# Kernel tuning notes

Measured on AMD Instinct MI355X. Metric: run time of the kernel, lower is better.

## Reference

```python
import jax, jax.numpy as jnp
import numpy as np

HEAD_DIM = 128
NUM_HEADS = 16
NUM_KV_HEADS = 16
ROPE_MAX_POS = 4096
ROPE_BASE = 10000.0


def _rope_tables(seq_len):
    # cos/sin cached tables: [S, D/2]
    inv_freq = 1.0 / (ROPE_BASE ** (jnp.arange(0, HEAD_DIM, 2, dtype=jnp.float32) / HEAD_DIM))
    t = jnp.arange(seq_len, dtype=jnp.float32)
    freqs = jnp.outer(t, inv_freq)
    return jnp.cos(freqs), jnp.sin(freqs)


def _apply_rope(x, cos, sin):
    # x: [B, S, H, D]; cos/sin: [S, D/2] -> broadcast over heads as [S, 1, D/2]
    orig_dtype = x.dtype
    c = cos[:, None, :]
    s = sin[:, None, :]
    xf = x.astype(jnp.float32)
    x_real, x_im = jnp.split(xf, 2, axis=-1)  # half-split (not interleaved) RoPE
    x_real_e = x_real * c - x_im * s
    x_im_e = x_im * c + x_real * s
    return jnp.concatenate((x_real_e, x_im_e), axis=-1).astype(orig_dtype)


def setup_inputs() -> dict:
    key = jax.random.key(0)
    k1, k2, k3 = jax.random.split(key, 3)
    B, S, H = 1, 4096, 2048
    hidden_states = jax.random.normal(k1, (B, S, H), dtype=jnp.float32)
    # trunc-normal-ish init, std ~ 1/sqrt(fan_in)
    w_qkv = jax.random.normal(k2, ((NUM_HEADS + 2 * NUM_KV_HEADS) * HEAD_DIM, H), dtype=jnp.float32) / jnp.sqrt(jnp.float32(H))
    w_o = jax.random.normal(k3, (H, NUM_HEADS * HEAD_DIM), dtype=jnp.float32) / jnp.sqrt(jnp.float32(NUM_HEADS * HEAD_DIM))
    return {"hidden_states": hidden_states, "w_qkv": w_qkv, "w_o": w_o}


def reference(hidden_states, w_qkv, w_o):
    B, S, _ = hidden_states.shape
    qkv = jnp.einsum('bsh,oh->bso', hidden_states, w_qkv)
    qkv = qkv.reshape(B, S, NUM_HEADS + 2 * NUM_KV_HEADS, HEAD_DIM)
    q = qkv[:, :, :NUM_HEADS]
    k = qkv[:, :, NUM_HEADS:NUM_HEADS + NUM_KV_HEADS]
    v = qkv[:, :, NUM_HEADS + NUM_KV_HEADS:]

    cos, sin = _rope_tables(S)
    q = _apply_rope(q, cos, sin)
    k = _apply_rope(k, cos, sin)

    scale = 1.0 / jnp.sqrt(jnp.float32(HEAD_DIM)).astype(q.dtype)
    # scores: [B, H, Sq, Sk]
    scores = jnp.einsum('bqhd,bkhd->bhqk', q, k) * scale
    causal = jnp.tril(jnp.ones((S, S), dtype=bool))
    scores = jnp.where(causal[None, None], scores, jnp.finfo(scores.dtype).min)
    probs = jax.nn.softmax(scores, axis=-1)
    attn = jnp.einsum('bhqk,bkhd->bqhd', probs, v)
    attn = attn.reshape(B, S, NUM_HEADS * HEAD_DIM)
    return jnp.einsum('bso,ho->bsh', attn, w_o)
```

## Files before the change

### kernel.cpp

```cpp
#include <hip/hip_runtime.h>

typedef __bf16 bf16;
typedef __bf16 bf16x8 __attribute__((ext_vector_type(8)));
typedef __bf16 bf16x4 __attribute__((ext_vector_type(4)));
typedef float f32x4 __attribute__((ext_vector_type(4)));

#define SEQ 4096
#define QKV_LD 6144
#define HNUM 16

__device__ __forceinline__ void async16(const bf16* g, bf16* l) {
    __builtin_amdgcn_global_load_lds((const __attribute__((address_space(1))) void*)g,
                                     (__attribute__((address_space(3))) void*)l, 16, 0, 0);
}

__global__ __launch_bounds__(256) void cast_f32_bf16(const float* __restrict__ src,
                                                     bf16* __restrict__ dst, int n) {
    int i = (blockIdx.x * 256 + threadIdx.x) * 8;
    if (i >= n) return;
    f32x4 a = *(const f32x4*)(src + i);
    f32x4 b = *(const f32x4*)(src + i + 4);
    bf16x8 w;
#pragma unroll
    for (int j = 0; j < 4; j++) { w[j] = (bf16)a[j]; w[4 + j] = (bf16)b[j]; }
    *(bf16x8*)(dst + i) = w;
}

template <int A_F32, int B_F32, int C_F32>
__global__ __launch_bounds__(256) void gemm_nt(const void* __restrict__ Ap,
                                               const void* __restrict__ Bp,
                                               void* __restrict__ Cp,
                                               int M, int N, int K) {
    __shared__ __align__(16) bf16 sA[128 * 32];
    __shared__ __align__(16) bf16 sB[128 * 32];
    const int tid  = threadIdx.x;
    const int wave = tid >> 6, lane = tid & 63;
    const int qd = lane >> 4, ln = lane & 15;
    const int bm = blockIdx.x * 128, bn = blockIdx.y * 128;
    const int wm = (wave >> 1) * 64, wn = (wave & 1) * 64;

    const int srow = wave * 16 + (lane >> 2);
    const int scol = (lane & 3) * 8;
    const size_t rowoff = (size_t)srow * K + scol;
    const size_t rowskip = (size_t)64 * K;

    const bf16* Ab = (const bf16*)Ap + (size_t)bm * K + rowoff;
    const bf16* Bb = (const bf16*)Bp + (size_t)bn * K + rowoff;
    const float* Af = (const float*)Ap + (size_t)bm * K + rowoff;
    const float* Bf = (const float*)Bp + (size_t)bn * K + rowoff;
    bf16* sAd0 = &sA[(wave * 16) * 32];
    bf16* sAd1 = &sA[(64 + wave * 16) * 32];
    bf16* sBd0 = &sB[(wave * 16) * 32];
    bf16* sBd1 = &sB[(64 + wave * 16) * 32];
    bf16* sAw0 = &sA[srow * 32 + scol];
    bf16* sAw1 = &sA[(64 + srow) * 32 + scol];
    bf16* sBw0 = &sB[srow * 32 + scol];
    bf16* sBw1 = &sB[(64 + srow) * 32 + scol];

    f32x4 acc[4][4] = {};
    for (int k0 = 0; k0 < K; k0 += 32) {
        if (A_F32) {
            f32x4 u0 = *(const f32x4*)(Af + k0);
            f32x4 u1 = *(const f32x4*)(Af + k0 + 4);
            f32x4 u2 = *(const f32x4*)(Af + rowskip + k0);
            f32x4 u3 = *(const f32x4*)(Af + rowskip + k0 + 4);
            bf16x8 w0, w1;
#pragma unroll
            for (int i = 0; i < 4; i++) { w0[i] = (bf16)u0[i]; w0[4 + i] = (bf16)u1[i];
                                          w1[i] = (bf16)u2[i]; w1[4 + i] = (bf16)u3[i]; }
            *(bf16x8*)sAw0 = w0;
            *(bf16x8*)sAw1 = w1;
        } else {
            async16(Ab + k0, sAd0);
            async16(Ab + rowskip + k0, sAd1);
        }
        if (B_F32) {
            f32x4 u0 = *(const f32x4*)(Bf + k0);
            f32x4 u1 = *(const f32x4*)(Bf + k0 + 4);
            f32x4 u2 = *(const f32x4*)(Bf + rowskip + k0);
            f32x4 u3 = *(const f32x4*)(Bf + rowskip + k0 + 4);
            bf16x8 w0, w1;
#pragma unroll
            for (int i = 0; i < 4; i++) { w0[i] = (bf16)u0[i]; w0[4 + i] = (bf16)u1[i];
                                          w1[i] = (bf16)u2[i]; w1[4 + i] = (bf16)u3[i]; }
            *(bf16x8*)sBw0 = w0;
            *(bf16x8*)sBw1 = w1;
        } else {
            async16(Bb + k0, sBd0);
            async16(Bb + rowskip + k0, sBd1);
        }
        __syncthreads();
        bf16x8 af[4], bfr[4];
#pragma unroll
        for (int i = 0; i < 4; i++)
            af[i] = *(const bf16x8*)&sA[(wm + i * 16 + ln) * 32 + qd * 8];
#pragma unroll
        for (int j = 0; j < 4; j++)
            bfr[j] = *(const bf16x8*)&sB[(wn + j * 16 + ln) * 32 + qd * 8];
#pragma unroll
        for (int i = 0; i < 4; i++)
#pragma unroll
            for (int j = 0; j < 4; j++)
                acc[i][j] = __builtin_amdgcn_mfma_f32_16x16x32_bf16(af[i], bfr[j], acc[i][j], 0, 0, 0);
        __syncthreads();
    }
    const size_t cbase = (size_t)(bm + wm + qd * 4) * N + (bn + wn + ln);
#pragma unroll
    for (int i = 0; i < 4; i++)
#pragma unroll
        for (int j = 0; j < 4; j++)
#pragma unroll
            for (int r = 0; r < 4; r++) {
                size_t idx = cbase + (size_t)(i * 16 + r) * N + j * 16;
                if (C_F32) ((float*)Cp)[idx] = acc[i][j][r];
                else       ((bf16*)Cp)[idx] = (bf16)acc[i][j][r];
            }
}

__global__ __launch_bounds__(256) void rope_table(float* __restrict__ T) {
    int i = blockIdx.x * 256 + threadIdx.x;
    int s = i >> 6, d = i & 63;
    float inv_freq = powf(10000.0f, -(float)d * (1.0f / 64.0f));
    float ang = (float)s * inv_freq;
    T[2 * i]     = cosf(ang);
    T[2 * i + 1] = sinf(ang);
}

__global__ __launch_bounds__(256) void rope_k_tab(bf16* __restrict__ QKV,
                                                  const float* __restrict__ T) {
    const int s  = blockIdx.x;
    const int t  = threadIdx.x;
    const int hh = (blockIdx.y << 2) + (t >> 6);
    const int d  = t & 63;
    bf16* p = QKV + (size_t)s * QKV_LD + hh * 128 + d;
    float2 cs = ((const float2*)T)[(size_t)s * 64 + d];
    float x0 = (float)p[0];
    float x1 = (float)p[64];
    p[0]  = (bf16)(x0 * cs.x - x1 * cs.y);
    p[64] = (bf16)(x1 * cs.x + x0 * cs.y);
}

__global__ __launch_bounds__(256) void rope_k_inline(bf16* __restrict__ QKV) {
    const int s  = blockIdx.x;
    const int t  = threadIdx.x;
    const int hh = (blockIdx.y << 2) + (t >> 6);
    const int d  = t & 63;
    bf16* p = QKV + (size_t)s * QKV_LD + hh * 128 + d;
    float x0 = (float)p[0];
    float x1 = (float)p[64];
    float inv_freq = powf(10000.0f, -(float)d * (1.0f / 64.0f));
    float ang = (float)s * inv_freq;
    float c = cosf(ang), sn = sinf(ang);
    p[0]  = (bf16)(x0 * c - x1 * sn);
    p[64] = (bf16)(x1 * c + x0 * sn);
}

__global__ __launch_bounds__(256) void transpose_v(const bf16* __restrict__ QKV,
                                                   bf16* __restrict__ VT) {
    __shared__ bf16 t[64][65];
    const int s0 = blockIdx.x * 64;
    const int d0 = blockIdx.y * 64;
    const int r = threadIdx.x >> 3, c = threadIdx.x & 7;
#pragma unroll
    for (int u = 0; u < 2; u++) {
        bf16x8 v = *(const bf16x8*)(QKV + (size_t)(s0 + u * 32 + r) * QKV_LD + 4096 + d0 + c * 8);
#pragma unroll
        for (int e = 0; e < 8; e++) t[u * 32 + r][c * 8 + e] = v[e];
    }
    __syncthreads();
#pragma unroll
    for (int u = 0; u < 2; u++) {
        bf16x8 w;
#pragma unroll
        for (int e = 0; e < 8; e++) w[e] = t[c * 8 + e][u * 32 + r];
        *(bf16x8*)(VT + (size_t)(d0 + u * 32 + r) * SEQ + s0 + c * 8) = w;
    }
}

template <int USE_VT>
__global__ __launch_bounds__(256, 2) void flash_attn(const bf16* __restrict__ QKV,
                                                     const bf16* __restrict__ VT,
                                                     bf16* __restrict__ O) {
    __shared__ __align__(16) bf16 sK[64 * 128];
    __shared__ __align__(16) bf16 sV[128 * 64];
    __shared__ __align__(16) bf16 sP[4][32 * 64];
    const int tid  = threadIdx.x;
    const int wave = tid >> 6, lane = tid & 63;
    const int qd = lane >> 4, ln = lane & 15;
    const int h  = blockIdx.x;
    const int qtile = 31 - blockIdx.y;
    const int qw0 = qtile * 128 + wave * 32;
    const int nkv = 2 * qtile + 2;
    const float scale = 0.08838834764831843f;

    bf16x8 Qf[2][4];
#pragma unroll
    for (int qt = 0; qt < 2; qt++) {
        const bf16* Qg = QKV + (size_t)(qw0 + qt * 16 + ln) * QKV_LD + h * 128;
#pragma unroll
        for (int ks = 0; ks < 4; ks++) {
            bf16x8 q8 = *(const bf16x8*)(Qg + ks * 32 + qd * 8);
#pragma unroll
            for (int e = 0; e < 8; e++) q8[e] = (bf16)((float)q8[e] * scale);
            Qf[qt][ks] = q8;
        }
    }

    f32x4 Oacc[2][8] = {};
    float l_i[2] = {0.0f, 0.0f};

    const int krow = tid >> 4;
    const int kblk = tid & 15;
    const int vrow = tid >> 3;
    const int vblk = tid & 7;
    const int vd   = tid & 127;
    const int vh   = tid >> 7;
    const bf16* Kg  = QKV + 2048 + h * 128;
    const bf16* Vg  = QKV + 4096 + h * 128;
    const bf16* VTg = VT + (size_t)h * 128 * SEQ;

    bf16x8 Kpre[4], Vpre[4];
#pragma unroll
    for (int rr = 0; rr < 4; rr++)
        Kpre[rr] = *(const bf16x8*)(Kg + (size_t)(rr * 16 + krow) * QKV_LD + kblk * 8);
    if (USE_VT) {
#pragma unroll
        for (int u = 0; u < 4; u++)
            Vpre[u] = *(const bf16x8*)(VTg + (size_t)(u * 32 + vrow) * SEQ + vblk * 8);
    } else {
#pragma unroll
        for (int u = 0; u < 4; u++)
#pragma unroll
            for (int j = 0; j < 8; j++)
                Vpre[u][j] = Vg[(size_t)(vh * 32 + u * 8 + j) * QKV_LD + vd];
    }

    for (int kt = 0; kt < nkv; kt++) {
        const int kbase = kt * 64;
#pragma unroll
        for (int rr = 0; rr < 4; rr++) {
            int kv = rr * 16 + krow;
            *(bf16x8*)&sK[kv * 128 + ((kblk ^ (kv & 7)) * 8)] = Kpre[rr];
        }
        if (USE_VT) {
#pragma unroll
            for (int u = 0; u < 4; u++) {
                int d = u * 32 + vrow;
                *(bf16x8*)&sV[d * 64 + ((vblk ^ (d & 7)) * 8)] = Vpre[u];
            }
        } else {
#pragma unroll
            for (int u = 0; u < 4; u++)
                *(bf16x8*)&sV[vd * 64 + (((vh * 4 + u) ^ (vd & 7)) * 8)] = Vpre[u];
        }
        __syncthreads();
        if (kt + 1 < nkv) {
            const int nb = kbase + 64;
#pragma unroll
            for (int rr = 0; rr < 4; rr++)
                Kpre[rr] = *(const bf16x8*)(Kg + (size_t)(nb + rr * 16 + krow) * QKV_LD + kblk * 8);
            if (USE_VT) {
#pragma unroll
                for (int u = 0; u < 4; u++)
                    Vpre[u] = *(const bf16x8*)(VTg + (size_t)(u * 32 + vrow) * SEQ + nb + vblk * 8);
            } else {
#pragma unroll
                for (int u = 0; u < 4; u++)
#pragma unroll
                    for (int j = 0; j < 8; j++)
                        Vpre[u][j] = Vg[(size_t)(nb + vh * 32 + u * 8 + j) * QKV_LD + vd];
            }
        }
        if (kbase <= qw0 + 31) {
            f32x4 Sacc[2][4] = {};
#pragma unroll
            for (int ks = 0; ks < 4; ks++)
#pragma unroll
                for (int j = 0; j < 4; j++) {
                    bf16x8 af = *(const bf16x8*)&sK[(j * 16 + ln) * 128 + (((ks * 4 + qd) ^ (ln & 7)) * 8)];
                    Sacc[0][j] = __builtin_amdgcn_mfma_f32_16x16x32_bf16(af, Qf[0][ks], Sacc[0][j], 0, 0, 0);
                    Sacc[1][j] = __builtin_amdgcn_mfma_f32_16x16x32_bf16(af, Qf[1][ks], Sacc[1][j], 0, 0, 0);
                }
#pragma unroll
            for (int qt = 0; qt < 2; qt++) {
                const int qs = qw0 + qt * 16;
                if (kbase + 63 > qs) {
#pragma unroll
                    for (int j = 0; j < 4; j++)
#pragma unroll
                        for (int r = 0; r < 4; r++)
                            if (kbase + j * 16 + qd * 4 + r > qs + ln) Sacc[qt][j][r] = -1e30f;
                }
                float psum = 0.0f;
#pragma unroll
                for (int j = 0; j < 4; j++) {
                    bf16x4 p4;
#pragma unroll
                    for (int r = 0; r < 4; r++) {
                        float p = __expf(Sacc[qt][j][r]);
                        psum += p;
                        p4[r] = (bf16)p;
                    }
                    int blk = (j * 2 + (qd >> 1)) ^ (ln & 7);
                    *(bf16x4*)&sP[wave][(qt * 16 + ln) * 64 + blk * 8 + (qd & 1) * 4] = p4;
                }
                psum += __shfl_xor(psum, 16);
                psum += __shfl_xor(psum, 32);
                l_i[qt] += psum;
            }
#pragma unroll
            for (int ks = 0; ks < 2; ks++) {
                bf16x8 pf0 = *(const bf16x8*)&sP[wave][(0 * 16 + ln) * 64 + (((ks * 4 + qd) ^ (ln & 7)) * 8)];
                bf16x8 pf1 = *(const bf16x8*)&sP[wave][(1 * 16 + ln) * 64 + (((ks * 4 + qd) ^ (ln & 7)) * 8)];
#pragma unroll
                for (int dt = 0; dt < 8; dt++) {
                    bf16x8 vf = *(const bf16x8*)&sV[(dt * 16 + ln) * 64 + (((ks * 4 + qd) ^ (ln & 7)) * 8)];
                    Oacc[0][dt] = __builtin_amdgcn_mfma_f32_16x16x32_bf16(pf0, vf, Oacc[0][dt], 0, 0, 0);
                    Oacc[1][dt] = __builtin_amdgcn_mfma_f32_16x16x32_bf16(pf1, vf, Oacc[1][dt], 0, 0, 0);
                }
            }
        }
        __syncthreads();
    }
#pragma unroll
    for (int qt = 0; qt < 2; qt++) {
        float linv[4];
#pragma unroll
        for (int r = 0; r < 4; r++)
            linv[r] = 1.0f / __shfl(l_i[qt], (lane & 48) | (qd * 4 + r));
        bf16* Ob = O + (size_t)(qw0 + qt * 16 + qd * 4) * 2048 + h * 128 + ln;
#pragma unroll
        for (int dt = 0; dt < 8; dt++)
#pragma unroll
            for (int r = 0; r < 4; r++)
                Ob[(size_t)r * 2048 + dt * 16] = (bf16)(Oacc[qt][dt][r] * linv[r]);
    }
}

extern "C" void kernel_launch(void* const* d_in, const int* in_sizes, int n_in,
                              void* d_out, int out_size, void* d_ws, size_t ws_size,
                              hipStream_t stream) {
    const float* X    = (const float*)d_in[0];
    const float* Wqkv = (const float*)d_in[1];
    const float* Wo   = (const float*)d_in[2];
    float* out = (float*)d_out;
    bf16* QKV = (bf16*)d_ws;
    bf16* ATT = QKV + (size_t)4096 * 6144;

    const size_t nX = (size_t)4096 * 2048, nWq = (size_t)6144 * 2048, nWo = (size_t)2048 * 2048;
    const size_t need = (nX * 3 + nWq * 2 + nWo) * 2 + nX * 2;

    if (ws_size >= need) {
        bf16* Xb  = ATT + nX;
        bf16* Wqb = Xb + nX;
        bf16* Wob = Wqb + nWq;
        bf16*  VT  = Xb;
        float* Tab = (float*)Wqb;
        cast_f32_bf16<<<(int)(nX  / 8 / 256), 256, 0, stream>>>(X, Xb, (int)nX);
        cast_f32_bf16<<<(int)(nWq / 8 / 256), 256, 0, stream>>>(Wqkv, Wqb, (int)nWq);
        cast_f32_bf16<<<(int)(nWo / 8 / 256), 256, 0, stream>>>(Wo, Wob, (int)nWo);
        gemm_nt<0, 0, 0><<<dim3(32, 48), 256, 0, stream>>>(Xb, Wqb, QKV, 4096, 6144, 2048);
        rope_table<<<1024, 256, 0, stream>>>(Tab);
        rope_k_tab<<<dim3(4096, 8), 256, 0, stream>>>(QKV, Tab);
        transpose_v<<<dim3(64, 32), 256, 0, stream>>>(QKV, VT);
        flash_attn<1><<<dim3(HNUM, 32), 256, 0, stream>>>(QKV, VT, ATT);
        gemm_nt<0, 0, 1><<<dim3(32, 16), 256, 0, stream>>>(ATT, Wob, out, 4096, 2048, 2048);
    } else {
        gemm_nt<1, 1, 0><<<dim3(32, 48), 256, 0, stream>>>(X, Wqkv, QKV, 4096, 6144, 2048);
        rope_k_inline<<<dim3(4096, 8), 256, 0, stream>>>(QKV);
        flash_attn<0><<<dim3(HNUM, 32), 256, 0, stream>>>(QKV, (const bf16*)nullptr, ATT);
        gemm_nt<0, 1, 1><<<dim3(32, 16), 256, 0, stream>>>(ATT, Wo, out, 4096, 2048, 2048);
    }
}
```

Baseline: 457.5 us.

## Replace QKV projection GEMM with 256x256-tile pipelined MFMA kernel

Adds a new bf16 GEMM kernel for the QKV projection. It uses 256x256 output tiles, 512 threads and a double-buffered LDS with XOR-swizzled async global-to-LDS loads. The K loop is split into phases that issue the next tile's loads alongside MFMA work, with explicit waitcnt, barriers and setprio scheduling. The goal is more data reuse per tile and better overlap of memory with compute. The costs are heavier LDS and register use, and a grid of only 384 blocks, which gives coarser work balancing across CUs.

```diff
diff --git a/kernel.cpp b/kernel.cpp
--- a/kernel.cpp
+++ b/kernel.cpp
@@ -24,6 +24,106 @@
 #pragma unroll
     for (int j = 0; j < 4; j++) { w[j] = (bf16)a[j]; w[4 + j] = (bf16)b[j]; }
     *(bf16x8*)(dst + i) = w;
+}
+
+
+__device__ __forceinline__ bf16x8 ldfrag(const bf16* slot, int row, int qd) {
+    int lin  = row * 64 + qd * 16;
+    int phys = lin ^ (((lin >> 9) & 1) << 5);
+    return *(const bf16x8*)((const char*)slot + phys);
+}
+
+#define STAGE2(SG, SGR0, STT, SKK, SBUF, SMAT)                                  \
+    {                                                                           \
+        int tcl = (STT) < NT ? (STT) : NT - 1;                                  \
+        const bf16* gsrc = (SG) + (size_t)(SGR0)*K + tcl * 64 + (SKK)*32;       \
+        bf16* sl = &LDS[SBUF][SMAT][SKK][0];                                    \
+        async16(gsrc + g0, (bf16*)((char*)sl + lb0));                           \
+        async16(gsrc + g1, (bf16*)((char*)sl + lb1));                           \
+    }
+
+#define PHASE(QM, KKI, LOADB, SG, SGR0, STT, SKK, SBUF, SMAT, DOVM)             \
+    {                                                                           \
+        if (LOADB) {                                                            \
+            _Pragma("unroll") for (int j = 0; j < 4; j++)                       \
+                bB[j] = ldfrag(&LDS[bi][1][KKI][0], wc * 64 + j * 16 + ln, qd); \
+        }                                                                       \
+        bf16x8 aA[4];                                                           \
+        _Pragma("unroll") for (int i = 0; i < 4; i++)                           \
+            aA[i] = ldfrag(&LDS[bi][0][KKI][0],                                 \
+                           wr * 128 + (QM)*64 + i * 16 + ln, qd);               \
+        STAGE2(SG, SGR0, STT, SKK, SBUF, SMAT);                                 \
+        __builtin_amdgcn_sched_barrier(0);                                      \
+        if (DOVM) {                                                             \
+            asm volatile("s_waitcnt vmcnt(4)" ::: "memory");                    \
+            __builtin_amdgcn_sched_barrier(0);                                  \
+        }                                                                       \
+        __builtin_amdgcn_s_barrier();                                           \
+        __builtin_amdgcn_sched_barrier(0);                                      \
+        __builtin_amdgcn_s_setprio(1);                                          \
+        _Pragma("unroll") for (int i = 0; i < 4; i++)                           \
+            _Pragma("unroll") for (int j = 0; j < 4; j++)                       \
+                acc[(QM)*4 + i][j] = __builtin_amdgcn_mfma_f32_16x16x32_bf16(   \
+                    aA[i], bB[j], acc[(QM)*4 + i][j], 0, 0, 0);                 \
+        __builtin_amdgcn_s_setprio(0);                                          \
+        __builtin_amdgcn_sched_barrier(0);                                      \
+        __builtin_amdgcn_s_barrier();                                           \
+        __builtin_amdgcn_sched_barrier(0);                                      \
+    }
+
+__global__ __launch_bounds__(512, 2) void gemm256_nt(const bf16* __restrict__ A,
+                                                     const bf16* __restrict__ B,
+                                                     bf16* __restrict__ C,
+                                                     int M, int N, int K) {
+    __shared__ __align__(16) bf16 LDS[2][2][2][256 * 32];
+    const int tid  = threadIdx.x;
+    const int wave = tid >> 6, lane = tid & 63;
+    const int qd = lane >> 4, ln = lane & 15;
+    const int wr = wave >> 2, wc = wave & 3;
+    const int bm = blockIdx.x * 256, bn = blockIdx.y * 256;
+    const int NT = K >> 6;
+
+    const int seg0 = wave * 2, seg1 = seg0 + 1;
+    const int Pr0 = seg0 * 1024 + lane * 16;
+    const int Pr1 = seg1 * 1024 + lane * 16;
+    const int Lr0 = Pr0 ^ (((Pr0 >> 9) & 1) << 5);
+    const int Lr1 = Pr1 ^ (((Pr1 >> 9) & 1) << 5);
+    const size_t g0 = (size_t)(Lr0 >> 6) * K + ((Lr0 & 63) >> 1);
+    const size_t g1 = (size_t)(Lr1 >> 6) * K + ((Lr1 & 63) >> 1);
+    const int lb0 = seg0 * 1024, lb1 = seg1 * 1024;
+
+    f32x4 acc[8][4] = {};
+
+    STAGE2(A, bm, 0, 0, 0, 0);
+    STAGE2(B, bn, 0, 0, 0, 1);
+    STAGE2(A, bm, 0, 1, 0, 0);
+    STAGE2(B, bn, 0, 1, 0, 1);
+    STAGE2(A, bm, 1, 0, 1, 0);
+    STAGE2(B, bn, 1, 0, 1, 1);
+    __builtin_amdgcn_sched_barrier(0);
+    asm volatile("s_waitcnt vmcnt(4)" ::: "memory");
+    __builtin_amdgcn_sched_barrier(0);
+    __builtin_amdgcn_s_barrier();
+    __builtin_amdgcn_sched_barrier(0);
+
+    for (int t = 0; t < NT; ++t) {
+        const int bi = t & 1;
+        bf16x8 bB[4];
+        PHASE(0, 0, 1, A, bm, t + 1, 1, bi ^ 1, 0, 0)
+        PHASE(1, 0, 0, B, bn, t + 1, 1, bi ^ 1, 1, 0)
+        PHASE(0, 1, 1, A, bm, t + 2, 0, bi,     0, 0)
+        PHASE(1, 1, 0, B, bn, t + 2, 0, bi,     1, 1)
+    }
+    asm volatile("s_waitcnt vmcnt(0)" ::: "memory");
+
+    const size_t cb = (size_t)(bm + wr * 128 + qd * 4) * N + (bn + wc * 64 + ln);
+#pragma unroll
+    for (int mi = 0; mi < 8; mi++)
+#pragma unroll
+        for (int j = 0; j < 4; j++)
+#pragma unroll
+            for (int r = 0; r < 4; r++)
+                C[cb + (size_t)(mi * 16 + r) * N + j * 16] = (bf16)acc[mi][j][r];
 }
 
 template <int A_F32, int B_F32, int C_F32>
@@ -359,7 +459,7 @@
         cast_f32_bf16<<<(int)(nX  / 8 / 256), 256, 0, stream>>>(X, Xb, (int)nX);
         cast_f32_bf16<<<(int)(nWq / 8 / 256), 256, 0, stream>>>(Wqkv, Wqb, (int)nWq);
         cast_f32_bf16<<<(int)(nWo / 8 / 256), 256, 0, stream>>>(Wo, Wob, (int)nWo);
-        gemm_nt<0, 0, 0><<<dim3(32, 48), 256, 0, stream>>>(Xb, Wqb, QKV, 4096, 6144, 2048);
+        gemm256_nt<<<dim3(16, 24), 512, 0, stream>>>(Xb, Wqb, QKV, 4096, 6144, 2048);
         rope_table<<<1024, 256, 0, stream>>>(Tab);
         rope_k_tab<<<dim3(4096, 8), 256, 0, stream>>>(QKV, Tab);
         transpose_v<<<dim3(64, 32), 256, 0, stream>>>(QKV, VT);
```

New measurement: 440.9 us. -3.6%, faster.
